# Kernel tuning notes

Hardware: AMD Instinct MI355X
Metric: run time of the kernel (lower is better)

The kernel has to match this reference:

```python
import jax, jax.numpy as jnp
import numpy as np

B, D, U = 8192, 2048, 2048  # batch rows, input dim, units
NB_FACTOR = 3
MASK_DENSITY = 1.0 / 16.0  # butterfly-like sparse factor density


def _glorot_uniform(key, shape):
    fan_in, fan_out = shape[0], shape[-1]
    limit = np.sqrt(6.0 / (fan_in + fan_out)).astype(np.float32)
    return jax.random.uniform(key, shape, jnp.float32, -limit, limit)


def setup_inputs() -> dict:
    key = jax.random.key(0)
    kx, km0, km1, km2, kk0, kk1, kk2, ks = jax.random.split(key, 8)
    x = jax.random.normal(kx, (B, D), jnp.float32)
    # Fixed sparsity patterns (constants, like K.constant sparsity_masks)
    m0 = (jax.random.uniform(km0, (D, U)) < MASK_DENSITY).astype(jnp.float32)
    m1 = (jax.random.uniform(km1, (U, U)) < MASK_DENSITY).astype(jnp.float32)
    m2 = (jax.random.uniform(km2, (U, U)) < MASK_DENSITY).astype(jnp.float32)
    k0 = _glorot_uniform(kk0, (D, U))
    k1 = _glorot_uniform(kk1, (U, U))
    k2 = _glorot_uniform(kk2, (U, U))
    scaling = _glorot_uniform(ks, (1,))  # scaler weight, shape (1,)
    bias = jnp.zeros((U,), jnp.float32)
    return {"x": x, "k0": k0, "k1": k1, "k2": k2,
            "m0": m0, "m1": m1, "m2": m2,
            "scaling": scaling, "bias": bias}


def reference(x, k0, k1, k2, m0, m1, m2, scaling, bias):
    # output = activation(scaling * (x @ (k0*m0) @ (k1*m1) @ (k2*m2)) + bias)
    out = x @ (k0 * m0)          # [B, U]
    out = out @ (k1 * m1)        # [B, U]
    out = out @ (k2 * m2)        # [B, U]
    out = scaling * out + bias   # scale then channels-last bias add
    return jax.nn.relu(out)
```

## Files before the change

### kernel.cpp

```cpp
#include <hip/hip_runtime.h>
#include <hip/hip_bf16.h>


typedef __attribute__((ext_vector_type(8)))  short  short8;
typedef __attribute__((ext_vector_type(8)))  ushort ushort8v;
typedef __attribute__((ext_vector_type(16))) float  f32x16;

#define KD 2048
#define ND 2048

__device__ __forceinline__ ushort f2b(float f) {
    union { float f; unsigned u; } v; v.f = f;
    unsigned r = v.u + 0x7fffu + ((v.u >> 16) & 1u);
    return (ushort)(r >> 16);
}

__device__ __forceinline__ void gload16(const ushort* g, ushort* l) {
    __builtin_amdgcn_global_load_lds(
        (const __attribute__((address_space(1))) void*)g,
        (__attribute__((address_space(3))) void*)l, 16, 0, 0);
}

__global__ __launch_bounds__(256)
void convx(const float* __restrict__ x, ushort* __restrict__ xb)
{
    const size_t i = (size_t)blockIdx.x * 256 + threadIdx.x;
    const float4* src = reinterpret_cast<const float4*>(x) + i * 2;
    const float4 f0 = src[0], f1 = src[1];
    ushort8v u;
    u[0]=f2b(f0.x); u[1]=f2b(f0.y); u[2]=f2b(f0.z); u[3]=f2b(f0.w);
    u[4]=f2b(f1.x); u[5]=f2b(f1.y); u[6]=f2b(f1.z); u[7]=f2b(f1.w);
    reinterpret_cast<ushort8v*>(xb)[i] = u;
}

__global__ __launch_bounds__(256)
void convT3(const float* __restrict__ k0w, const float* __restrict__ k1w,
            const float* __restrict__ k2w, const float* __restrict__ m0w,
            const float* __restrict__ m1w, const float* __restrict__ m2w,
            ushort* __restrict__ wbT)
{
    const int z = blockIdx.z;
    const float* kw = z == 0 ? k0w : (z == 1 ? k1w : k2w);
    const float* mw = z == 0 ? m0w : (z == 1 ? m1w : m2w);
    ushort* o = wbT + (size_t)z * KD * ND;

    __shared__ ushort t[32][36];
    const int tid = threadIdx.x;
    const int bk = blockIdx.x * 32, bn = blockIdx.y * 32;
    {
        const int r = tid >> 3, c = (tid & 7) * 4;
        const size_t g = (size_t)(bk + r) * ND + bn + c;
        const float4 kv = *reinterpret_cast<const float4*>(kw + g);
        const float4 mv = *reinterpret_cast<const float4*>(mw + g);
        t[r][c + 0] = f2b(kv.x * mv.x);
        t[r][c + 1] = f2b(kv.y * mv.y);
        t[r][c + 2] = f2b(kv.z * mv.z);
        t[r][c + 3] = f2b(kv.w * mv.w);
    }
    __syncthreads();
    {
        const int n = tid >> 3, kq = (tid & 7) * 4;
        ushort4 ov;
        ov.x = t[kq + 0][n]; ov.y = t[kq + 1][n];
        ov.z = t[kq + 2][n]; ov.w = t[kq + 3][n];
        *reinterpret_cast<ushort4*>(&o[(size_t)(bn + n) * KD + bk + kq]) = ov;
    }
}

template<int EPI>
__global__ __launch_bounds__(512, 2)
void gemm256(const ushort* __restrict__ A, const ushort* __restrict__ BT,
             void* __restrict__ Cout,
             const float* __restrict__ scaling, const float* __restrict__ bias)
{
    __shared__ ushort S[2][2][2][256 * 32];

    const int tid  = threadIdx.x;
    const int lane = tid & 63;
    const int wid  = tid >> 6;
    const int wr   = wid >> 2, wc = wid & 3;
    const int l31  = lane & 31;
    const int lh   = lane >> 5;
    const int rk   = (l31 >> 1) & 3;
    const int id   = blockIdx.x;
    const int swz  = (id & 7) * 32 + (id >> 3);
    const int bn   = (swz & 7) * 256;
    const int bm   = (swz >> 3) * 256;
    const int srow = lane >> 2;
    const int wrow = wid * 32;
    const int ssw  = ((lane & 3) ^ ((srow >> 1) & 3)) * 8;

    f32x16 acc[4][2] = {};

#define STAGE(op, bufl, kh, tile, G, g0) do {                                        \
    gload16(G + (size_t)((g0) + wrow + srow)      * KD + (tile)*64 + (kh)*32 + ssw,  \
            &S[bufl][op][kh][(wrow)      * 32]);                                     \
    gload16(G + (size_t)((g0) + wrow + 16 + srow) * KD + (tile)*64 + (kh)*32 + ssw,  \
            &S[bufl][op][kh][(wrow + 16) * 32]);                                     \
  } while (0)

#define BAR()  asm volatile("s_barrier" ::: "memory")
#define VM4()  asm volatile("s_waitcnt vmcnt(4)" ::: "memory")
#define VM0()  asm volatile("s_waitcnt vmcnt(0)" ::: "memory")
#define LGK0() asm volatile("s_waitcnt lgkmcnt(0)" ::: "memory")
#define SB()   __builtin_amdgcn_sched_barrier(0)
#define PRI1() __builtin_amdgcn_s_setprio(1)
#define PRI0() __builtin_amdgcn_s_setprio(0)

#define FA32(bufl, kh, mt, ks) (*(const short8*)&S[bufl][0][kh][ \
        (wr*128 + (mt)*32 + l31)*32 + ((((ks)*2 + lh) ^ rk) * 8)])
#define FB32(bufl, kh, nt, ks) (*(const short8*)&S[bufl][1][kh][ \
        (wc*64  + (nt)*32 + l31)*32 + ((((ks)*2 + lh) ^ rk) * 8)])

#define MF(a_, b_, c_) __builtin_amdgcn_mfma_f32_32x32x16_bf16(a_, b_, c_, 0, 0, 0)

#define PH(bufl, kh, STG, GATE) do {                                                  \
    short8 a00=FA32(bufl,kh,0,0), a10=FA32(bufl,kh,1,0),                              \
           a20=FA32(bufl,kh,2,0), a30=FA32(bufl,kh,3,0);                              \
    short8 a01=FA32(bufl,kh,0,1), a11=FA32(bufl,kh,1,1),                              \
           a21=FA32(bufl,kh,2,1), a31=FA32(bufl,kh,3,1);                              \
    short8 b00=FB32(bufl,kh,0,0), b10=FB32(bufl,kh,1,0);                              \
    short8 b01=FB32(bufl,kh,0,1), b11=FB32(bufl,kh,1,1);                              \
    STG; BAR(); SB(); PRI1();                                                         \
    acc[0][0]=MF(b00,a00,acc[0][0]); acc[1][0]=MF(b00,a10,acc[1][0]);                 \
    acc[2][0]=MF(b00,a20,acc[2][0]); acc[3][0]=MF(b00,a30,acc[3][0]);                 \
    acc[0][1]=MF(b10,a00,acc[0][1]); acc[1][1]=MF(b10,a10,acc[1][1]);                 \
    acc[2][1]=MF(b10,a20,acc[2][1]); acc[3][1]=MF(b10,a30,acc[3][1]);                 \
    acc[0][0]=MF(b01,a01,acc[0][0]); acc[1][0]=MF(b01,a11,acc[1][0]);                 \
    acc[2][0]=MF(b01,a21,acc[2][0]); acc[3][0]=MF(b01,a31,acc[3][0]);                 \
    acc[0][1]=MF(b11,a01,acc[0][1]); acc[1][1]=MF(b11,a11,acc[1][1]);                 \
    acc[2][1]=MF(b11,a21,acc[2][1]); acc[3][1]=MF(b11,a31,acc[3][1]);                 \
    PRI0(); SB(); LGK0(); GATE; BAR();                                                \
  } while (0)

    STAGE(0, 0, 0, 0, A,  bm); STAGE(1, 0, 0, 0, BT, bn);
    STAGE(0, 0, 1, 0, A,  bm); STAGE(1, 0, 1, 0, BT, bn);
    STAGE(1, 1, 0, 1, BT, bn); STAGE(0, 1, 0, 1, A,  bm);
    VM4();
    BAR();

    const int NITER = KD / 128;
    for (int it = 0; it < NITER - 1; ++it) {
        const int t1 = 2 * it + 1, t2 = 2 * it + 2, t3 = 2 * it + 3;
        PH(0, 0, STAGE(1,1,1,t1,BT,bn); STAGE(0,1,1,t1,A,bm), );
        PH(0, 1, STAGE(1,0,0,t2,BT,bn); STAGE(0,0,0,t2,A,bm), VM4());
        PH(1, 0, STAGE(1,0,1,t2,BT,bn); STAGE(0,0,1,t2,A,bm), );
        PH(1, 1, STAGE(1,1,0,t3,BT,bn); STAGE(0,1,0,t3,A,bm), VM4());
    }
    PH(0, 0, STAGE(1,1,1,31,BT,bn); STAGE(0,1,1,31,A,bm), );
    PH(0, 1, , VM0());
    PH(1, 0, , );
    PH(1, 1, , );

    const float sc = EPI ? scaling[0] : 0.f;
#pragma unroll
    for (int mt = 0; mt < 4; ++mt) {
        const size_t grow = (size_t)(bm + wr * 128 + mt * 32 + l31);
#pragma unroll
        for (int nt = 0; nt < 2; ++nt) {
#pragma unroll
            for (int r = 0; r < 4; ++r) {
                const int gcol = bn + wc * 64 + nt * 32 + lh * 4 + r * 8;
                if constexpr (EPI) {
                    const float4 bv = *reinterpret_cast<const float4*>(bias + gcol);
                    float4 v;
                    v.x = fmaxf(fmaf(sc, acc[mt][nt][4*r+0], bv.x), 0.f);
                    v.y = fmaxf(fmaf(sc, acc[mt][nt][4*r+1], bv.y), 0.f);
                    v.z = fmaxf(fmaf(sc, acc[mt][nt][4*r+2], bv.z), 0.f);
                    v.w = fmaxf(fmaf(sc, acc[mt][nt][4*r+3], bv.w), 0.f);
                    *reinterpret_cast<float4*>((float*)Cout + grow * ND + gcol) = v;
                } else {
                    ushort4 v;
                    v.x = f2b(acc[mt][nt][4*r+0]); v.y = f2b(acc[mt][nt][4*r+1]);
                    v.z = f2b(acc[mt][nt][4*r+2]); v.w = f2b(acc[mt][nt][4*r+3]);
                    *reinterpret_cast<ushort4*>((ushort*)Cout + grow * ND + gcol) = v;
                }
            }
        }
    }
#undef STAGE
#undef PH
#undef MF
#undef FA32
#undef FB32
}

extern "C" void kernel_launch(void* const* d_in, const int* in_sizes, int n_in,
                              void* d_out, int out_size, void* d_ws, size_t ws_size,
                              hipStream_t stream)
{
    const float* x    = (const float*)d_in[0];
    const float* k0w  = (const float*)d_in[1];
    const float* k1w  = (const float*)d_in[2];
    const float* k2w  = (const float*)d_in[3];
    const float* m0w  = (const float*)d_in[4];
    const float* m1w  = (const float*)d_in[5];
    const float* m2w  = (const float*)d_in[6];
    const float* sc   = (const float*)d_in[7];
    const float* bias = (const float*)d_in[8];

    const int Md = in_sizes[0] / KD;
    const size_t NE = (size_t)Md * KD;

    ushort* act1 = (ushort*)d_out;
    ushort* xb   = (ushort*)d_out + NE;
    float*  out  = (float*)d_out;
    ushort* act2 = (ushort*)d_ws;
    ushort* wbT  = (ushort*)d_ws + NE;

    dim3 bl(256);
    dim3 gX(NE / (256 * 8));
    dim3 gT(KD / 32, ND / 32, 3);
    dim3 gG((ND / 256) * (Md / 256)), bG(512);

    convx <<<gX, bl, 0, stream>>>(x, xb);
    convT3<<<gT, bl, 0, stream>>>(k0w, k1w, k2w, m0w, m1w, m2w, wbT);

    gemm256<0><<<gG, bG, 0, stream>>>(xb,   wbT,                     act1, nullptr, nullptr);
    gemm256<0><<<gG, bG, 0, stream>>>(act1, wbT + (size_t)KD * ND,     act2, nullptr, nullptr);
    gemm256<1><<<gG, bG, 0, stream>>>(act2, wbT + (size_t)2 * KD * ND, out,  sc, bias);
}
```

Measured before the change: 262.1 us.

## Restructure GEMM main loop to full-K64 double buffer with one barrier per tile

The shared-memory layout changes from split 32-wide K halves to full 64-wide K rows, with an 8-way XOR swizzle. The four-phase pipeline, which used partial vmcnt waits and a barrier on each side of every phase, becomes a simple double-buffered loop. Each iteration issues the next tile's loads during two compute sub-phases and ends with a single full wait and barrier. This cuts barrier and scheduling overhead. The cost is shallower prefetch: loads are drained fully each tile, so load latency may be exposed and stall the MFMA pipe.

New measurement: 238.7 us. 8.9% less time.

```diff
diff --git a/kernel.cpp b/kernel.cpp
--- a/kernel.cpp
+++ b/kernel.cpp
@@ -73,7 +73,7 @@
              void* __restrict__ Cout,
              const float* __restrict__ scaling, const float* __restrict__ bias)
 {
-    __shared__ ushort S[2][2][2][256 * 32];
+    __shared__ ushort S[2][2][256 * 64];
 
     const int tid  = threadIdx.x;
     const int lane = tid & 63;
@@ -81,76 +81,73 @@
     const int wr   = wid >> 2, wc = wid & 3;
     const int l31  = lane & 31;
     const int lh   = lane >> 5;
-    const int rk   = (l31 >> 1) & 3;
     const int id   = blockIdx.x;
     const int swz  = (id & 7) * 32 + (id >> 3);
     const int bn   = (swz & 7) * 256;
     const int bm   = (swz >> 3) * 256;
-    const int srow = lane >> 2;
+    const int srow = lane >> 3;
     const int wrow = wid * 32;
-    const int ssw  = ((lane & 3) ^ ((srow >> 1) & 3)) * 8;
+    const int ssw  = ((lane & 7) ^ (srow & 7)) * 8;
+    const int rk3  = l31 & 7;
 
     f32x16 acc[4][2] = {};
 
-#define STAGE(op, bufl, kh, tile, G, g0) do {                                        \
-    gload16(G + (size_t)((g0) + wrow + srow)      * KD + (tile)*64 + (kh)*32 + ssw,  \
-            &S[bufl][op][kh][(wrow)      * 32]);                                     \
-    gload16(G + (size_t)((g0) + wrow + 16 + srow) * KD + (tile)*64 + (kh)*32 + ssw,  \
-            &S[bufl][op][kh][(wrow + 16) * 32]);                                     \
+#define STAGE32(op, bufl, tile, G, g0) do {                                          \
+    gload16(G + (size_t)((g0) + wrow +  0 + srow) * KD + (tile)*64 + ssw,            \
+            &S[bufl][op][(wrow +  0) * 64]);                                         \
+    gload16(G + (size_t)((g0) + wrow +  8 + srow) * KD + (tile)*64 + ssw,            \
+            &S[bufl][op][(wrow +  8) * 64]);                                         \
+    gload16(G + (size_t)((g0) + wrow + 16 + srow) * KD + (tile)*64 + ssw,            \
+            &S[bufl][op][(wrow + 16) * 64]);                                         \
+    gload16(G + (size_t)((g0) + wrow + 24 + srow) * KD + (tile)*64 + ssw,            \
+            &S[bufl][op][(wrow + 24) * 64]);                                         \
   } while (0)
 
 #define BAR()  asm volatile("s_barrier" ::: "memory")
-#define VM4()  asm volatile("s_waitcnt vmcnt(4)" ::: "memory")
 #define VM0()  asm volatile("s_waitcnt vmcnt(0)" ::: "memory")
 #define LGK0() asm volatile("s_waitcnt lgkmcnt(0)" ::: "memory")
-#define SB()   __builtin_amdgcn_sched_barrier(0)
 #define PRI1() __builtin_amdgcn_s_setprio(1)
 #define PRI0() __builtin_amdgcn_s_setprio(0)
 
-#define FA32(bufl, kh, mt, ks) (*(const short8*)&S[bufl][0][kh][ \
-        (wr*128 + (mt)*32 + l31)*32 + ((((ks)*2 + lh) ^ rk) * 8)])
-#define FB32(bufl, kh, nt, ks) (*(const short8*)&S[bufl][1][kh][ \
-        (wc*64  + (nt)*32 + l31)*32 + ((((ks)*2 + lh) ^ rk) * 8)])
-
-#define MF(a_, b_, c_) __builtin_amdgcn_mfma_f32_32x32x16_bf16(a_, b_, c_, 0, 0, 0)
-
-#define PH(bufl, kh, STG, GATE) do {                                                  \
-    short8 a00=FA32(bufl,kh,0,0), a10=FA32(bufl,kh,1,0),                              \
-           a20=FA32(bufl,kh,2,0), a30=FA32(bufl,kh,3,0);                              \
-    short8 a01=FA32(bufl,kh,0,1), a11=FA32(bufl,kh,1,1),                              \
-           a21=FA32(bufl,kh,2,1), a31=FA32(bufl,kh,3,1);                              \
-    short8 b00=FB32(bufl,kh,0,0), b10=FB32(bufl,kh,1,0);                              \
-    short8 b01=FB32(bufl,kh,0,1), b11=FB32(bufl,kh,1,1);                              \
-    STG; BAR(); SB(); PRI1();                                                         \
-    acc[0][0]=MF(b00,a00,acc[0][0]); acc[1][0]=MF(b00,a10,acc[1][0]);                 \
-    acc[2][0]=MF(b00,a20,acc[2][0]); acc[3][0]=MF(b00,a30,acc[3][0]);                 \
-    acc[0][1]=MF(b10,a00,acc[0][1]); acc[1][1]=MF(b10,a10,acc[1][1]);                 \
-    acc[2][1]=MF(b10,a20,acc[2][1]); acc[3][1]=MF(b10,a30,acc[3][1]);                 \
-    acc[0][0]=MF(b01,a01,acc[0][0]); acc[1][0]=MF(b01,a11,acc[1][0]);                 \
-    acc[2][0]=MF(b01,a21,acc[2][0]); acc[3][0]=MF(b01,a31,acc[3][0]);                 \
-    acc[0][1]=MF(b11,a01,acc[0][1]); acc[1][1]=MF(b11,a11,acc[1][1]);                 \
-    acc[2][1]=MF(b11,a21,acc[2][1]); acc[3][1]=MF(b11,a31,acc[3][1]);                 \
-    PRI0(); SB(); LGK0(); GATE; BAR();                                                \
+#define FA32(bufl, mt, ks) (*(const short8*)&S[bufl][0][                              \
+        (wr*128 + (mt)*32 + l31)*64 + ((((ks)*2 + lh) ^ rk3) * 8)])
+#define FB32(bufl, nt, ks) (*(const short8*)&S[bufl][1][                              \
+        (wc*64  + (nt)*32 + l31)*64 + ((((ks)*2 + lh) ^ rk3) * 8)])
+
+#define MF32(a_, b_, c_) __builtin_amdgcn_mfma_f32_32x32x16_bf16(a_, b_, c_, 0, 0, 0)
+
+#define SUBPH(bufl, ka, kb, STG) do {                                                 \
+    short8 b0a = FB32(bufl,0,ka), b1a = FB32(bufl,1,ka);                              \
+    short8 a0a = FA32(bufl,0,ka), a1a = FA32(bufl,1,ka),                              \
+           a2a = FA32(bufl,2,ka), a3a = FA32(bufl,3,ka);                              \
+    short8 b0b = FB32(bufl,0,kb), b1b = FB32(bufl,1,kb);                              \
+    short8 a0b = FA32(bufl,0,kb), a1b = FA32(bufl,1,kb),                              \
+           a2b = FA32(bufl,2,kb), a3b = FA32(bufl,3,kb);                              \
+    STG;                                                                              \
+    PRI1();                                                                           \
+    acc[0][0]=MF32(b0a,a0a,acc[0][0]); acc[0][1]=MF32(b1a,a0a,acc[0][1]);             \
+    acc[1][0]=MF32(b0a,a1a,acc[1][0]); acc[1][1]=MF32(b1a,a1a,acc[1][1]);             \
+    acc[2][0]=MF32(b0a,a2a,acc[2][0]); acc[2][1]=MF32(b1a,a2a,acc[2][1]);             \
+    acc[3][0]=MF32(b0a,a3a,acc[3][0]); acc[3][1]=MF32(b1a,a3a,acc[3][1]);             \
+    acc[0][0]=MF32(b0b,a0b,acc[0][0]); acc[0][1]=MF32(b1b,a0b,acc[0][1]);             \
+    acc[1][0]=MF32(b0b,a1b,acc[1][0]); acc[1][1]=MF32(b1b,a1b,acc[1][1]);             \
+    acc[2][0]=MF32(b0b,a2b,acc[2][0]); acc[2][1]=MF32(b1b,a2b,acc[2][1]);             \
+    acc[3][0]=MF32(b0b,a3b,acc[3][0]); acc[3][1]=MF32(b1b,a3b,acc[3][1]);             \
+    PRI0();                                                                           \
   } while (0)
 
-    STAGE(0, 0, 0, 0, A,  bm); STAGE(1, 0, 0, 0, BT, bn);
-    STAGE(0, 0, 1, 0, A,  bm); STAGE(1, 0, 1, 0, BT, bn);
-    STAGE(1, 1, 0, 1, BT, bn); STAGE(0, 1, 0, 1, A,  bm);
-    VM4();
+    STAGE32(0, 0, 0, A, bm); STAGE32(1, 0, 0, BT, bn);
+    VM0();
     BAR();
 
-    const int NITER = KD / 128;
-    for (int it = 0; it < NITER - 1; ++it) {
-        const int t1 = 2 * it + 1, t2 = 2 * it + 2, t3 = 2 * it + 3;
-        PH(0, 0, STAGE(1,1,1,t1,BT,bn); STAGE(0,1,1,t1,A,bm), );
-        PH(0, 1, STAGE(1,0,0,t2,BT,bn); STAGE(0,0,0,t2,A,bm), VM4());
-        PH(1, 0, STAGE(1,0,1,t2,BT,bn); STAGE(0,0,1,t2,A,bm), );
-        PH(1, 1, STAGE(1,1,0,t3,BT,bn); STAGE(0,1,0,t3,A,bm), VM4());
-    }
-    PH(0, 0, STAGE(1,1,1,31,BT,bn); STAGE(0,1,1,31,A,bm), );
-    PH(0, 1, , VM0());
-    PH(1, 0, , );
-    PH(1, 1, , );
+    for (int t = 0; t < 31; ++t) {
+        const int bf = t & 1;
+        SUBPH(bf, 0, 1, STAGE32(0, bf ^ 1, t + 1, A,  bm));
+        SUBPH(bf, 2, 3, STAGE32(1, bf ^ 1, t + 1, BT, bn));
+        LGK0(); VM0(); BAR();
+    }
+    SUBPH(1, 0, 1, );
+    SUBPH(1, 2, 3, );
 
     const float sc = EPI ? scaling[0] : 0.f;
 #pragma unroll
@@ -178,9 +175,9 @@
             }
         }
     }
-#undef STAGE
-#undef PH
-#undef MF
+#undef STAGE32
+#undef SUBPH
+#undef MF32
 #undef FA32
 #undef FB32
 }
```
